# Kernel optimization log

Measured on AMD Instinct MI355X. Metric: run time of the kernel, lower is better.

The kernel has to match this reference:

```python
import jax, jax.numpy as jnp
import numpy as np

PATCH = 7
STRIDE = 1


def extract_patches(im, p=PATCH, stride=STRIDE):
    # im: [b, c, h, w] -> patches [b, N, c*p*p] (torch.nn.Unfold-style layout)
    pt = jax.lax.conv_general_dilated_patches(
        im, filter_shape=(p, p), window_strides=(stride, stride), padding='VALID')
    # pt: [b, c*p*p, h', w']
    b, d = pt.shape[0], pt.shape[1]
    return pt.reshape(b, d, -1).transpose(0, 2, 1)  # [b, N, d]


def coherence_swd(xp, yp, rand):
    # xp, yp: [N, d]; rand: [d, P]
    r = rand / jnp.std(rand, axis=0, keepdims=True, ddof=1)  # torch.std is unbiased
    px = xp @ r  # [N, P]
    py = yp @ r  # [N, P]
    ix = jnp.argsort(px, axis=0).T  # [P, N]
    iy = jnp.argsort(py, axis=0).T  # [P, N]
    # Gather full patch vectors by per-projection sorted order, L1 distance.
    # xp[ix]: [P, N, d] -- the big irregular-gather intermediate.
    diff = jnp.abs(xp[ix] - yp[iy])  # [P, N, d]
    # loss = (1/P) * sum_p mean(|...|_p); each term has identical size -> plain mean
    return diff.mean()


def setup_inputs() -> dict:
    key = jax.random.key(0)
    k1, k2, k3 = jax.random.split(key, 3)
    b, c, h, w = 1, 3, 96, 96
    d = c * PATCH * PATCH  # 147
    num_proj = 256
    x = jax.random.normal(k1, (b, c, h, w), dtype=jnp.float32)
    y = jax.random.normal(k2, (b, c, h, w), dtype=jnp.float32)
    rand = jax.random.normal(k3, (d, num_proj), dtype=jnp.float32)
    return {"x": x, "y": y, "rand": rand}


def reference(x, y, rand):
    x_patches = extract_patches(x)  # [b, N, d]
    y_patches = extract_patches(y)
    losses = jax.vmap(coherence_swd, in_axes=(0, 0, None))(x_patches, y_patches, rand)  # [b]
    return losses.mean()  # batch_reduction='mean'
```

## Files before the change

### kernel.cpp

```cpp
#include <hip/hip_runtime.h>

#define HH 96
#define WW 96
#define OH 90
#define OW 90
#define NPATCH 8100
#define DD 147
#define NPROJ 256
#define TN 64
#define KPAD 160
#define NKS 5
#define SORT_T 512
#define NBUCK 4096
#define KPT 16
#define PGRP 16
#define NCH 64
#define KPB2 128
#define QSCALE 21.25f

typedef short bf16x8 __attribute__((ext_vector_type(8)));
typedef float f32x4 __attribute__((ext_vector_type(4)));

__device__ __forceinline__ unsigned short bf16_rne(float f) {
    unsigned u = __builtin_bit_cast(unsigned, f);
    u += 0x7FFFu + ((u >> 16) & 1u);
    return (unsigned short)(u >> 16);
}
__device__ __forceinline__ float bf16_f(unsigned short h) {
    return __builtin_bit_cast(float, (unsigned)h << 16);
}

__device__ __forceinline__ unsigned sad4(unsigned x, unsigned y, unsigned a) {
    unsigned d;
    asm("v_sad_u8 %0, %1, %2, %3" : "=v"(d) : "v"(x), "v"(y), "v"(a));
    return d;
}

__global__ __launch_bounds__(512, 2)
void patch_proj_kernel(const float* __restrict__ x, const float* __restrict__ y,
                       const float* __restrict__ rnd,
                       int* __restrict__ xm8, int* __restrict__ ym8,
                       int* __restrict__ xt8, int* __restrict__ yt8,
                       float* __restrict__ pxT, float* __restrict__ pyT,
                       float* __restrict__ out)
{
    __shared__ unsigned short sh[2][TN * KPAD];
    const int tid = threadIdx.x;
    const int n0 = blockIdx.x * TN;
    const int img = blockIdx.y;
    const float* __restrict__ src = img ? y : x;
    int* __restrict__ m8 = img ? ym8 : xm8;
    int* __restrict__ t8 = img ? yt8 : xt8;
    float* __restrict__ pT = img ? pyT : pxT;
    if (blockIdx.x == 0 && img == 0 && tid == 0) out[0] = 0.0f;

    const int wv = tid >> 6, lane = tid & 63;
    const int cl = lane & 15, qk = lane >> 4;

    bf16x8 bh[NKS][2], bl[NKS][2];
#pragma unroll
    for (int ks = 0; ks < NKS; ++ks) {
#pragma unroll
        for (int nt = 0; nt < 2; ++nt) {
            const int col = wv * 32 + nt * 16 + cl;
#pragma unroll
            for (int j = 0; j < 8; ++j) {
                const int k = ks * 32 + qk * 8 + j;
                const float v = (k < DD) ? rnd[k * NPROJ + col] : 0.f;
                const unsigned short h = bf16_rne(v);
                bh[ks][nt][j] = (short)h;
                bl[ks][nt][j] = (short)bf16_rne(v - bf16_f(h));
            }
        }
    }

    for (int idx = tid; idx < TN * 40; idx += 512) {
        const int t = idx / 40;
        const int u = idx - t * 40;
        const int n = n0 + t;
        const int d0 = 4 * u;
        unsigned short h4[4], l4[4];
#pragma unroll
        for (int e = 0; e < 4; ++e) {
            const int d = d0 + e;
            float v = 0.f;
            if (n < NPATCH && d < DD) {
                const int oy = n / OW, ox = n - oy * OW;
                const int c  = d / 49, r  = d - c * 49;
                const int di = r / 7,  dj = r - di * 7;
                v = src[c * (HH * WW) + (oy + di) * WW + (ox + dj)];
            }
            const unsigned short hi = bf16_rne(v);
            h4[e] = hi;
            l4[e] = bf16_rne(v - bf16_f(hi));
        }
        const int mt = t >> 4, r16 = t & 15;
        const int ks = d0 >> 5, q = (d0 & 31) >> 3, jb = d0 & 7;
        const int fidx = (((mt * NKS + ks) * 4 + q) * 16 + r16) * 8 + jb;
        ushort4 hv; hv.x = h4[0]; hv.y = h4[1]; hv.z = h4[2]; hv.w = h4[3];
        ushort4 lv; lv.x = l4[0]; lv.y = l4[1]; lv.z = l4[2]; lv.w = l4[3];
        *(ushort4*)&sh[0][fidx] = hv;
        *(ushort4*)&sh[1][fidx] = lv;
        if (n < NPATCH) {
            unsigned w = 0;
#pragma unroll
            for (int e = 0; e < 4; ++e) {
                float f = fmaf(bf16_f(h4[e]), QSCALE, 128.5f);
                f = fminf(fmaxf(f, 0.f), 255.f);
                w |= ((unsigned)f) << (8 * e);
            }
            if (u < 32) m8[(size_t)n * 32 + u] = (int)w;
            else        t8[(size_t)n * 8 + (u - 32)] = (int)w;
        }
    }
    __syncthreads();

    f32x4 acc[4][2];
#pragma unroll
    for (int mt = 0; mt < 4; ++mt)
#pragma unroll
        for (int nt = 0; nt < 2; ++nt)
            acc[mt][nt] = (f32x4){0.f, 0.f, 0.f, 0.f};

#pragma unroll
    for (int ks = 0; ks < NKS; ++ks) {
#pragma unroll
        for (int mt = 0; mt < 4; ++mt) {
            const int base = ((mt * NKS + ks) * 64 + lane) * 8;
            const bf16x8 ah = *(const bf16x8*)&sh[0][base];
            const bf16x8 al = *(const bf16x8*)&sh[1][base];
#pragma unroll
            for (int nt = 0; nt < 2; ++nt) {
                acc[mt][nt] = __builtin_amdgcn_mfma_f32_16x16x32_bf16(ah, bh[ks][nt], acc[mt][nt], 0, 0, 0);
                acc[mt][nt] = __builtin_amdgcn_mfma_f32_16x16x32_bf16(ah, bl[ks][nt], acc[mt][nt], 0, 0, 0);
                acc[mt][nt] = __builtin_amdgcn_mfma_f32_16x16x32_bf16(al, bh[ks][nt], acc[mt][nt], 0, 0, 0);
            }
        }
    }

#pragma unroll
    for (int mt = 0; mt < 4; ++mt) {
        const int patch = n0 + mt * 16 + qk * 4;
#pragma unroll
        for (int nt = 0; nt < 2; ++nt) {
            const int proj = wv * 32 + nt * 16 + cl;
            float* rowp = pT + (size_t)proj * NPATCH + patch;
            if (patch + 3 < NPATCH) {
                *(f32x4*)rowp = acc[mt][nt];
            } else {
#pragma unroll
                for (int e = 0; e < 4; ++e)
                    if (patch + e < NPATCH) rowp[e] = acc[mt][nt][e];
            }
        }
    }
}

__global__ __launch_bounds__(SORT_T, 4)
void rank_kernel(const float* __restrict__ pT,
                 unsigned short* __restrict__ rxOut,
                 unsigned short* __restrict__ iyOut)
{
    __shared__ unsigned hist[NBUCK];
    __shared__ unsigned cnt[NBUCK];
    __shared__ float    skey[8192];
    __shared__ unsigned wsum[8];
    const int pb = blockIdx.x;
    const int tid = threadIdx.x;
    const int lane = tid & 63;
    const float* col = pT + (size_t)pb * NPATCH;

    {
        uint4 z = make_uint4(0, 0, 0, 0);
        ((uint4*)hist)[tid] = z;
        ((uint4*)hist)[tid + SORT_T] = z;
    }
    __syncthreads();

    float k[KPT];
    int bk[KPT];
#pragma unroll
    for (int t = 0; t < KPT; ++t) {
        const int i = tid + SORT_T * t;
        if (i < NPATCH) {
            const float v = col[i];
            k[t] = v;
            int b = (int)((v + 51.2f) * 40.0f);
            b = b < 0 ? 0 : (b > NBUCK - 1 ? NBUCK - 1 : b);
            bk[t] = b;
            atomicAdd(&hist[b], 1u);
        } else {
            k[t] = 0.f;
            bk[t] = -1;
        }
    }
    __syncthreads();

    {
        const int b0 = tid * 8;
        unsigned h[8];
#pragma unroll
        for (int q = 0; q < 8; ++q) h[q] = hist[b0 + q];
        unsigned tsum = 0;
#pragma unroll
        for (int q = 0; q < 8; ++q) tsum += h[q];
        unsigned acc = tsum;
#pragma unroll
        for (int d = 1; d < 64; d <<= 1) {
            const unsigned v = __shfl_up(acc, d, 64);
            if (lane >= d) acc += v;
        }
        const unsigned wexcl = acc - tsum;
        if (lane == 63) wsum[tid >> 6] = acc;
        __syncthreads();
        if (tid == 0) {
            unsigned roff = 0;
#pragma unroll
            for (int w = 0; w < 8; ++w) {
                const unsigned tt = wsum[w];
                wsum[w] = roff;
                roff += tt;
            }
        }
        __syncthreads();
        unsigned run = wsum[tid >> 6] + wexcl;
#pragma unroll
        for (int q = 0; q < 8; ++q) { cnt[b0 + q] = run; run += h[q]; }
    }
    __syncthreads();

#pragma unroll
    for (int t = 0; t < KPT; ++t) {
        if (bk[t] >= 0) {
            const unsigned pos = atomicAdd(&cnt[bk[t]], 1u);
            skey[pos] = k[t];
        }
    }
    __syncthreads();

#pragma unroll
    for (int t = 0; t < KPT; ++t) {
        const int i = tid + SORT_T * t;
        if (bk[t] < 0) continue;
        const int b = bk[t];
        const unsigned end = cnt[b];
        const unsigned cb = hist[b];
        const unsigned start = end - cb;
        const float myk = k[t];
        unsigned r = start;
        for (unsigned s2 = start; s2 < end; ++s2)
            r += (skey[s2] < myk) ? 1u : 0u;
        if (pb < NPROJ)
            rxOut[(size_t)pb * NPATCH + i] = (unsigned short)r;
        else
            iyOut[(size_t)(pb - NPROJ) * NPATCH + r] = (unsigned short)i;
    }
}

__global__ __launch_bounds__(256, 4)
void reduce_kernel(const uint4* __restrict__ xm8, const uint4* __restrict__ ym8,
                   const uint4* __restrict__ xt8, const uint4* __restrict__ yt8,
                   const unsigned short* __restrict__ rx,
                   const unsigned short* __restrict__ iy,
                   float* __restrict__ out)
{
    __shared__ unsigned short sp[PGRP * KPB2];
    const int p0 = blockIdx.y * PGRP;
    const int i0 = blockIdx.x * KPB2;
    const int iend = min(i0 + KPB2, NPATCH);
    const int tid = threadIdx.x;
    const int wave = tid >> 6, lane = tid & 63;

    for (int idx = tid; idx < PGRP * KPB2; idx += 256) {
        const int pp = idx >> 7, r = idx & 127;
        int src = i0 + r;
        src = src < NPATCH ? src : NPATCH - 1;
        const int p = p0 + pp;
        const unsigned short rk = rx[(size_t)p * NPATCH + src];
        const unsigned short j = iy[(size_t)p * NPATCH + rk];
        sp[idx] = j < NPATCH ? j : (unsigned short)(NPATCH - 1);
    }
    __syncthreads();

    unsigned uacc = 0;

    {
        const int g = lane >> 3;
        const int u = lane & 7;
#pragma unroll
        for (int it = 0; it < 4; ++it) {
            const int i = i0 + wave * 8 + it * 32;
            const uint4 xa = xm8[(size_t)i * 8 + lane];
            int jj[PGRP];
#pragma unroll
            for (int pp = 0; pp < PGRP; ++pp)
                jj[pp] = sp[pp * KPB2 + (i - i0) + g];
            uint4 ya[PGRP];
#pragma unroll
            for (int pp = 0; pp < PGRP; ++pp)
                ya[pp] = ym8[(size_t)jj[pp] * 8 + u];
            unsigned s0 = 0, s1 = 0;
#pragma unroll
            for (int pp = 0; pp < PGRP; ++pp) {
                s0 = sad4(xa.x, ya[pp].x, s0);
                s1 = sad4(xa.y, ya[pp].y, s1);
                s0 = sad4(xa.z, ya[pp].z, s0);
                s1 = sad4(xa.w, ya[pp].w, s1);
            }
            uacc += (i + g < iend) ? (s0 + s1) : 0u;
        }
    }

    {
        const int g2 = lane >> 1;
        const int u2 = lane & 1;
        const int i2 = i0 + wave * 32;
        const uint4 xa = xt8[(size_t)i2 * 2 + lane];
        int jj[PGRP];
#pragma unroll
        for (int pp = 0; pp < PGRP; ++pp)
            jj[pp] = sp[pp * KPB2 + (i2 - i0) + g2];
        uint4 ya[PGRP];
#pragma unroll
        for (int pp = 0; pp < PGRP; ++pp)
            ya[pp] = yt8[(size_t)jj[pp] * 2 + u2];
        unsigned s0 = 0, s1 = 0;
#pragma unroll
        for (int pp = 0; pp < PGRP; ++pp) {
            s0 = sad4(xa.x, ya[pp].x, s0);
            s1 = sad4(xa.y, ya[pp].y, s1);
            s0 = sad4(xa.z, ya[pp].z, s0);
            s1 = sad4(xa.w, ya[pp].w, s1);
        }
        uacc += (i2 + g2 < iend) ? (s0 + s1) : 0u;
    }

    float facc = (float)uacc;
#pragma unroll
    for (int o = 32; o > 0; o >>= 1) facc += __shfl_down(facc, o, 64);

    __shared__ float sred[4];
    if (lane == 0) sred[wave] = facc;
    __syncthreads();
    if (tid == 0) {
        const float s = sred[0] + sred[1] + sred[2] + sred[3];
        const float scale = (float)(1.0 / ((double)NPROJ * (double)NPATCH *
                                           (double)DD * (double)QSCALE));
        atomicAdd(out, s * scale);
    }
}

extern "C" void kernel_launch(void* const* d_in, const int* in_sizes, int n_in,
                              void* d_out, int out_size, void* d_ws, size_t ws_size,
                              hipStream_t stream)
{
    const float* x   = (const float*)d_in[0];
    const float* y   = (const float*)d_in[1];
    const float* rnd = (const float*)d_in[2];

    char* ws = (char*)d_ws;
    int* xm8 = (int*)(ws + 0);
    int* ym8 = (int*)(ws + 1036800);
    int* xt8 = (int*)(ws + 2073600);
    int* yt8 = (int*)(ws + 2332800);
    float* pxT = (float*)(ws + 2592000);
    float* pyT = (float*)(ws + 10886400);
    unsigned short* rx = (unsigned short*)(ws + 19180800);
    unsigned short* iy = (unsigned short*)(ws + 23328000);
    float* out = (float*)d_out;

    hipLaunchKernelGGL(patch_proj_kernel, dim3((NPATCH + TN - 1) / TN, 2), dim3(512), 0, stream,
                       x, y, rnd, xm8, ym8, xt8, yt8, pxT, pyT, out);
    hipLaunchKernelGGL(rank_kernel, dim3(2 * NPROJ), dim3(SORT_T), 0, stream,
                       pxT, rx, iy);
    hipLaunchKernelGGL(reduce_kernel, dim3(NCH, NPROJ / PGRP), dim3(256), 0, stream,
                       (const uint4*)xm8, (const uint4*)ym8,
                       (const uint4*)xt8, (const uint4*)yt8, rx, iy, out);
}
```

Baseline: 126.9 us.

## Fuse three kernels into one cooperative persistent kernel with grid syncs

Replaces the separate projection, ranking and reduction launches with a single cooperative kernel of 256 blocks that separates the phases with grid-wide syncs and reuses one shared-memory union across them. It also adds a pre-pass that converts the random projection matrix into split-bf16 transposed buffers once, instead of every projection block reconverting it. The aim is to remove launch gaps and redundant per-block conversion. In exchange, the ranking and reduction phases each loop twice per block, the kernel pays for three grid barriers, and the shared union sized for the ranking phase may limit occupancy.

```diff
diff --git a/kernel.cpp b/kernel.cpp
--- a/kernel.cpp
+++ b/kernel.cpp
@@ -1,4 +1,7 @@
 #include <hip/hip_runtime.h>
+#include <hip/hip_cooperative_groups.h>
+
+namespace cg = cooperative_groups;
 
 #define HH 96
 #define WW 96
@@ -17,6 +20,7 @@
 #define NCH 64
 #define KPB2 128
 #define QSCALE 21.25f
+#define GRID_B 256
 
 typedef short bf16x8 __attribute__((ext_vector_type(8)));
 typedef float f32x4 __attribute__((ext_vector_type(4)));
@@ -36,317 +40,335 @@
     return d;
 }
 
+union SmemU {
+    struct { unsigned short sh[2][TN * KPAD]; } a;
+    struct { unsigned hist[NBUCK]; unsigned cnt[NBUCK];
+             float skey[8192]; unsigned wsum[8]; } b;
+    struct { unsigned short sp[2][PGRP * KPB2]; float sred[2][4]; } c;
+};
+
 __global__ __launch_bounds__(512, 2)
-void patch_proj_kernel(const float* __restrict__ x, const float* __restrict__ y,
-                       const float* __restrict__ rnd,
-                       int* __restrict__ xm8, int* __restrict__ ym8,
-                       int* __restrict__ xt8, int* __restrict__ yt8,
-                       float* __restrict__ pxT, float* __restrict__ pyT,
-                       float* __restrict__ out)
+void fused_swd(const float* __restrict__ x, const float* __restrict__ y,
+               const float* __restrict__ rnd,
+               unsigned short* __restrict__ rth, unsigned short* __restrict__ rtl,
+               int* __restrict__ xm8, int* __restrict__ ym8,
+               int* __restrict__ xt8, int* __restrict__ yt8,
+               float* __restrict__ pxT, float* __restrict__ pyT,
+               unsigned short* __restrict__ rx, unsigned short* __restrict__ iy,
+               float* __restrict__ out)
 {
-    __shared__ unsigned short sh[2][TN * KPAD];
+    __shared__ SmemU smem;
+    cg::grid_group grid = cg::this_grid();
+    const int b = blockIdx.x;
     const int tid = threadIdx.x;
-    const int n0 = blockIdx.x * TN;
-    const int img = blockIdx.y;
-    const float* __restrict__ src = img ? y : x;
-    int* __restrict__ m8 = img ? ym8 : xm8;
-    int* __restrict__ t8 = img ? yt8 : xt8;
-    float* __restrict__ pT = img ? pyT : pxT;
-    if (blockIdx.x == 0 && img == 0 && tid == 0) out[0] = 0.0f;
-
     const int wv = tid >> 6, lane = tid & 63;
     const int cl = lane & 15, qk = lane >> 4;
 
-    bf16x8 bh[NKS][2], bl[NKS][2];
-#pragma unroll
-    for (int ks = 0; ks < NKS; ++ks) {
-#pragma unroll
-        for (int nt = 0; nt < 2; ++nt) {
-            const int col = wv * 32 + nt * 16 + cl;
-#pragma unroll
-            for (int j = 0; j < 8; ++j) {
-                const int k = ks * 32 + qk * 8 + j;
-                const float v = (k < DD) ? rnd[k * NPROJ + col] : 0.f;
-                const unsigned short h = bf16_rne(v);
-                bh[ks][nt][j] = (short)h;
-                bl[ks][nt][j] = (short)bf16_rne(v - bf16_f(h));
-            }
-        }
+    {
+        const int idx = b * 512 + tid;
+        if (idx < NPROJ * KPAD) {
+            const int p = idx / KPAD;
+            const int k = idx - p * KPAD;
+            const float v = (k < DD) ? rnd[k * NPROJ + p] : 0.f;
+            const unsigned short hi = bf16_rne(v);
+            rth[idx] = hi;
+            rtl[idx] = bf16_rne(v - bf16_f(hi));
+        }
+        if (b == 0 && tid == 0) out[0] = 0.0f;
     }
-
-    for (int idx = tid; idx < TN * 40; idx += 512) {
-        const int t = idx / 40;
-        const int u = idx - t * 40;
-        const int n = n0 + t;
-        const int d0 = 4 * u;
-        unsigned short h4[4], l4[4];
-#pragma unroll
-        for (int e = 0; e < 4; ++e) {
-            const int d = d0 + e;
-            float v = 0.f;
-            if (n < NPATCH && d < DD) {
-                const int oy = n / OW, ox = n - oy * OW;
-                const int c  = d / 49, r  = d - c * 49;
-                const int di = r / 7,  dj = r - di * 7;
-                v = src[c * (HH * WW) + (oy + di) * WW + (ox + dj)];
-            }
-            const unsigned short hi = bf16_rne(v);
-            h4[e] = hi;
-            l4[e] = bf16_rne(v - bf16_f(hi));
-        }
-        const int mt = t >> 4, r16 = t & 15;
-        const int ks = d0 >> 5, q = (d0 & 31) >> 3, jb = d0 & 7;
-        const int fidx = (((mt * NKS + ks) * 4 + q) * 16 + r16) * 8 + jb;
-        ushort4 hv; hv.x = h4[0]; hv.y = h4[1]; hv.z = h4[2]; hv.w = h4[3];
-        ushort4 lv; lv.x = l4[0]; lv.y = l4[1]; lv.z = l4[2]; lv.w = l4[3];
-        *(ushort4*)&sh[0][fidx] = hv;
-        *(ushort4*)&sh[1][fidx] = lv;
-        if (n < NPATCH) {
-            unsigned w = 0;
+    grid.sync();
+
+    if (b < 254) {
+        const int img = b & 1;
+        const int n0 = (b >> 1) * TN;
+        const float* __restrict__ src = img ? y : x;
+        int* __restrict__ m8 = img ? ym8 : xm8;
+        int* __restrict__ t8 = img ? yt8 : xt8;
+        float* __restrict__ pT = img ? pyT : pxT;
+
+        bf16x8 bh[NKS][2], bl[NKS][2];
+#pragma unroll
+        for (int ks = 0; ks < NKS; ++ks) {
+#pragma unroll
+            for (int nt = 0; nt < 2; ++nt) {
+                const int col = wv * 32 + nt * 16 + cl;
+                const int k0 = ks * 32 + qk * 8;
+                bh[ks][nt] = *(const bf16x8*)&rth[col * KPAD + k0];
+                bl[ks][nt] = *(const bf16x8*)&rtl[col * KPAD + k0];
+            }
+        }
+
+        for (int idx = tid; idx < TN * 40; idx += 512) {
+            const int t = idx / 40;
+            const int u = idx - t * 40;
+            const int n = n0 + t;
+            const int d0 = 4 * u;
+            unsigned short h4[4], l4[4];
 #pragma unroll
             for (int e = 0; e < 4; ++e) {
-                float f = fmaf(bf16_f(h4[e]), QSCALE, 128.5f);
-                f = fminf(fmaxf(f, 0.f), 255.f);
-                w |= ((unsigned)f) << (8 * e);
-            }
-            if (u < 32) m8[(size_t)n * 32 + u] = (int)w;
-            else        t8[(size_t)n * 8 + (u - 32)] = (int)w;
+                const int d = d0 + e;
+                float v = 0.f;
+                if (n < NPATCH && d < DD) {
+                    const int oy = n / OW, ox = n - oy * OW;
+                    const int c  = d / 49, r  = d - c * 49;
+                    const int di = r / 7,  dj = r - di * 7;
+                    v = src[c * (HH * WW) + (oy + di) * WW + (ox + dj)];
+                }
+                const unsigned short hi = bf16_rne(v);
+                h4[e] = hi;
+                l4[e] = bf16_rne(v - bf16_f(hi));
+            }
+            const int mt = t >> 4, r16 = t & 15;
+            const int ks = d0 >> 5, q = (d0 & 31) >> 3, jb = d0 & 7;
+            const int fidx = (((mt * NKS + ks) * 4 + q) * 16 + r16) * 8 + jb;
+            ushort4 hv; hv.x = h4[0]; hv.y = h4[1]; hv.z = h4[2]; hv.w = h4[3];
+            ushort4 lv; lv.x = l4[0]; lv.y = l4[1]; lv.z = l4[2]; lv.w = l4[3];
+            *(ushort4*)&smem.a.sh[0][fidx] = hv;
+            *(ushort4*)&smem.a.sh[1][fidx] = lv;
+            if (n < NPATCH) {
+                unsigned w = 0;
+#pragma unroll
+                for (int e = 0; e < 4; ++e) {
+                    float f = fmaf(bf16_f(h4[e]), QSCALE, 128.5f);
+                    f = fminf(fmaxf(f, 0.f), 255.f);
+                    w |= ((unsigned)f) << (8 * e);
+                }
+                if (u < 32) m8[(size_t)n * 32 + u] = (int)w;
+                else        t8[(size_t)n * 8 + (u - 32)] = (int)w;
+            }
+        }
+        __syncthreads();
+
+        f32x4 acc[4][2];
+#pragma unroll
+        for (int mt = 0; mt < 4; ++mt)
+#pragma unroll
+            for (int nt = 0; nt < 2; ++nt)
+                acc[mt][nt] = (f32x4){0.f, 0.f, 0.f, 0.f};
+
+#pragma unroll
+        for (int ks = 0; ks < NKS; ++ks) {
+#pragma unroll
+            for (int mt = 0; mt < 4; ++mt) {
+                const int base = ((mt * NKS + ks) * 64 + lane) * 8;
+                const bf16x8 ah = *(const bf16x8*)&smem.a.sh[0][base];
+                const bf16x8 al = *(const bf16x8*)&smem.a.sh[1][base];
+#pragma unroll
+                for (int nt = 0; nt < 2; ++nt) {
+                    acc[mt][nt] = __builtin_amdgcn_mfma_f32_16x16x32_bf16(ah, bh[ks][nt], acc[mt][nt], 0, 0, 0);
+                    acc[mt][nt] = __builtin_amdgcn_mfma_f32_16x16x32_bf16(ah, bl[ks][nt], acc[mt][nt], 0, 0, 0);
+                    acc[mt][nt] = __builtin_amdgcn_mfma_f32_16x16x32_bf16(al, bh[ks][nt], acc[mt][nt], 0, 0, 0);
+                }
+            }
+        }
+
+#pragma unroll
+        for (int mt = 0; mt < 4; ++mt) {
+            const int patch = n0 + mt * 16 + qk * 4;
+#pragma unroll
+            for (int nt = 0; nt < 2; ++nt) {
+                const int proj = wv * 32 + nt * 16 + cl;
+                float* rowp = pT + (size_t)proj * NPATCH + patch;
+                if (patch + 3 < NPATCH) {
+                    *(f32x4*)rowp = acc[mt][nt];
+                } else {
+#pragma unroll
+                    for (int e = 0; e < 4; ++e)
+                        if (patch + e < NPATCH) rowp[e] = acc[mt][nt][e];
+                }
+            }
         }
     }
-    __syncthreads();
-
-    f32x4 acc[4][2];
-#pragma unroll
-    for (int mt = 0; mt < 4; ++mt)
-#pragma unroll
-        for (int nt = 0; nt < 2; ++nt)
-            acc[mt][nt] = (f32x4){0.f, 0.f, 0.f, 0.f};
-
-#pragma unroll
-    for (int ks = 0; ks < NKS; ++ks) {
-#pragma unroll
-        for (int mt = 0; mt < 4; ++mt) {
-            const int base = ((mt * NKS + ks) * 64 + lane) * 8;
-            const bf16x8 ah = *(const bf16x8*)&sh[0][base];
-            const bf16x8 al = *(const bf16x8*)&sh[1][base];
-#pragma unroll
-            for (int nt = 0; nt < 2; ++nt) {
-                acc[mt][nt] = __builtin_amdgcn_mfma_f32_16x16x32_bf16(ah, bh[ks][nt], acc[mt][nt], 0, 0, 0);
-                acc[mt][nt] = __builtin_amdgcn_mfma_f32_16x16x32_bf16(ah, bl[ks][nt], acc[mt][nt], 0, 0, 0);
-                acc[mt][nt] = __builtin_amdgcn_mfma_f32_16x16x32_bf16(al, bh[ks][nt], acc[mt][nt], 0, 0, 0);
-            }
-        }
+    grid.sync();
+
+    for (int rep = 0; rep < 2; ++rep) {
+        const int pb = b + rep * GRID_B;
+        const float* col = pxT + (size_t)pb * NPATCH;
+
+        {
+            uint4 z = make_uint4(0, 0, 0, 0);
+            ((uint4*)smem.b.hist)[tid] = z;
+            ((uint4*)smem.b.hist)[tid + SORT_T] = z;
+        }
+        __syncthreads();
+
+        float k[KPT];
+        int bk[KPT];
+#pragma unroll
+        for (int t = 0; t < KPT; ++t) {
+            const int i = tid + SORT_T * t;
+            if (i < NPATCH) {
+                const float v = col[i];
+                k[t] = v;
+                int bq = (int)((v + 51.2f) * 40.0f);
+                bq = bq < 0 ? 0 : (bq > NBUCK - 1 ? NBUCK - 1 : bq);
+                bk[t] = bq;
+                atomicAdd(&smem.b.hist[bq], 1u);
+            } else {
+                k[t] = 0.f;
+                bk[t] = -1;
+            }
+        }
+        __syncthreads();
+
+        {
+            const int b0 = tid * 8;
+            unsigned h[8];
+#pragma unroll
+            for (int q = 0; q < 8; ++q) h[q] = smem.b.hist[b0 + q];
+            unsigned tsum = 0;
+#pragma unroll
+            for (int q = 0; q < 8; ++q) tsum += h[q];
+            unsigned acc = tsum;
+#pragma unroll
+            for (int d = 1; d < 64; d <<= 1) {
+                const unsigned v = __shfl_up(acc, d, 64);
+                if (lane >= d) acc += v;
+            }
+            const unsigned wexcl = acc - tsum;
+            if (lane == 63) smem.b.wsum[tid >> 6] = acc;
+            __syncthreads();
+            if (tid == 0) {
+                unsigned roff = 0;
+#pragma unroll
+                for (int w = 0; w < 8; ++w) {
+                    const unsigned tt = smem.b.wsum[w];
+                    smem.b.wsum[w] = roff;
+                    roff += tt;
+                }
+            }
+            __syncthreads();
+            unsigned run = smem.b.wsum[tid >> 6] + wexcl;
+#pragma unroll
+            for (int q = 0; q < 8; ++q) { smem.b.cnt[b0 + q] = run; run += h[q]; }
+        }
+        __syncthreads();
+
+#pragma unroll
+        for (int t = 0; t < KPT; ++t) {
+            if (bk[t] >= 0) {
+                const unsigned pos = atomicAdd(&smem.b.cnt[bk[t]], 1u);
+                smem.b.skey[pos] = k[t];
+            }
+        }
+        __syncthreads();
+
+#pragma unroll
+        for (int t = 0; t < KPT; ++t) {
+            const int i = tid + SORT_T * t;
+            if (bk[t] < 0) continue;
+            const int bq = bk[t];
+            const unsigned end = smem.b.cnt[bq];
+            const unsigned cb = smem.b.hist[bq];
+            const unsigned start = end - cb;
+            const float myk = k[t];
+            unsigned r = start;
+            for (unsigned s2 = start; s2 < end; ++s2)
+                r += (smem.b.skey[s2] < myk) ? 1u : 0u;
+            if (pb < NPROJ)
+                rx[(size_t)pb * NPATCH + i] = (unsigned short)r;
+            else
+                iy[(size_t)(pb - NPROJ) * NPATCH + r] = (unsigned short)i;
+        }
+        __syncthreads();
     }
-
-#pragma unroll
-    for (int mt = 0; mt < 4; ++mt) {
-        const int patch = n0 + mt * 16 + qk * 4;
-#pragma unroll
-        for (int nt = 0; nt < 2; ++nt) {
-            const int proj = wv * 32 + nt * 16 + cl;
-            float* rowp = pT + (size_t)proj * NPATCH + patch;
-            if (patch + 3 < NPATCH) {
-                *(f32x4*)rowp = acc[mt][nt];
-            } else {
-#pragma unroll
-                for (int e = 0; e < 4; ++e)
-                    if (patch + e < NPATCH) rowp[e] = acc[mt][nt][e];
-            }
-        }
-    }
-}
-
-__global__ __launch_bounds__(SORT_T, 4)
-void rank_kernel(const float* __restrict__ pT,
-                 unsigned short* __restrict__ rxOut,
-                 unsigned short* __restrict__ iyOut)
-{
-    __shared__ unsigned hist[NBUCK];
-    __shared__ unsigned cnt[NBUCK];
-    __shared__ float    skey[8192];
-    __shared__ unsigned wsum[8];
-    const int pb = blockIdx.x;
-    const int tid = threadIdx.x;
-    const int lane = tid & 63;
-    const float* col = pT + (size_t)pb * NPATCH;
+    grid.sync();
 
     {
-        uint4 z = make_uint4(0, 0, 0, 0);
-        ((uint4*)hist)[tid] = z;
-        ((uint4*)hist)[tid + SORT_T] = z;
-    }
-    __syncthreads();
-
-    float k[KPT];
-    int bk[KPT];
-#pragma unroll
-    for (int t = 0; t < KPT; ++t) {
-        const int i = tid + SORT_T * t;
-        if (i < NPATCH) {
-            const float v = col[i];
-            k[t] = v;
-            int b = (int)((v + 51.2f) * 40.0f);
-            b = b < 0 ? 0 : (b > NBUCK - 1 ? NBUCK - 1 : b);
-            bk[t] = b;
-            atomicAdd(&hist[b], 1u);
-        } else {
-            k[t] = 0.f;
-            bk[t] = -1;
-        }
-    }
-    __syncthreads();
-
-    {
-        const int b0 = tid * 8;
-        unsigned h[8];
-#pragma unroll
-        for (int q = 0; q < 8; ++q) h[q] = hist[b0 + q];
-        unsigned tsum = 0;
-#pragma unroll
-        for (int q = 0; q < 8; ++q) tsum += h[q];
-        unsigned acc = tsum;
-#pragma unroll
-        for (int d = 1; d < 64; d <<= 1) {
-            const unsigned v = __shfl_up(acc, d, 64);
-            if (lane >= d) acc += v;
-        }
-        const unsigned wexcl = acc - tsum;
-        if (lane == 63) wsum[tid >> 6] = acc;
-        __syncthreads();
-        if (tid == 0) {
-            unsigned roff = 0;
-#pragma unroll
-            for (int w = 0; w < 8; ++w) {
-                const unsigned tt = wsum[w];
-                wsum[w] = roff;
-                roff += tt;
-            }
-        }
-        __syncthreads();
-        unsigned run = wsum[tid >> 6] + wexcl;
-#pragma unroll
-        for (int q = 0; q < 8; ++q) { cnt[b0 + q] = run; run += h[q]; }
-    }
-    __syncthreads();
-
-#pragma unroll
-    for (int t = 0; t < KPT; ++t) {
-        if (bk[t] >= 0) {
-            const unsigned pos = atomicAdd(&cnt[bk[t]], 1u);
-            skey[pos] = k[t];
-        }
-    }
-    __syncthreads();
-
-#pragma unroll
-    for (int t = 0; t < KPT; ++t) {
-        const int i = tid + SORT_T * t;
-        if (bk[t] < 0) continue;
-        const int b = bk[t];
-        const unsigned end = cnt[b];
-        const unsigned cb = hist[b];
-        const unsigned start = end - cb;
-        const float myk = k[t];
-        unsigned r = start;
-        for (unsigned s2 = start; s2 < end; ++s2)
-            r += (skey[s2] < myk) ? 1u : 0u;
-        if (pb < NPROJ)
-            rxOut[(size_t)pb * NPATCH + i] = (unsigned short)r;
-        else
-            iyOut[(size_t)(pb - NPROJ) * NPATCH + r] = (unsigned short)i;
-    }
-}
-
-__global__ __launch_bounds__(256, 4)
-void reduce_kernel(const uint4* __restrict__ xm8, const uint4* __restrict__ ym8,
-                   const uint4* __restrict__ xt8, const uint4* __restrict__ yt8,
-                   const unsigned short* __restrict__ rx,
-                   const unsigned short* __restrict__ iy,
-                   float* __restrict__ out)
-{
-    __shared__ unsigned short sp[PGRP * KPB2];
-    const int p0 = blockIdx.y * PGRP;
-    const int i0 = blockIdx.x * KPB2;
-    const int iend = min(i0 + KPB2, NPATCH);
-    const int tid = threadIdx.x;
-    const int wave = tid >> 6, lane = tid & 63;
-
-    for (int idx = tid; idx < PGRP * KPB2; idx += 256) {
-        const int pp = idx >> 7, r = idx & 127;
-        int src = i0 + r;
-        src = src < NPATCH ? src : NPATCH - 1;
-        const int p = p0 + pp;
-        const unsigned short rk = rx[(size_t)p * NPATCH + src];
-        const unsigned short j = iy[(size_t)p * NPATCH + rk];
-        sp[idx] = j < NPATCH ? j : (unsigned short)(NPATCH - 1);
-    }
-    __syncthreads();
-
-    unsigned uacc = 0;
-
-    {
-        const int g = lane >> 3;
-        const int u = lane & 7;
-#pragma unroll
-        for (int it = 0; it < 4; ++it) {
-            const int i = i0 + wave * 8 + it * 32;
-            const uint4 xa = xm8[(size_t)i * 8 + lane];
-            int jj[PGRP];
-#pragma unroll
-            for (int pp = 0; pp < PGRP; ++pp)
-                jj[pp] = sp[pp * KPB2 + (i - i0) + g];
-            uint4 ya[PGRP];
-#pragma unroll
-            for (int pp = 0; pp < PGRP; ++pp)
-                ya[pp] = ym8[(size_t)jj[pp] * 8 + u];
-            unsigned s0 = 0, s1 = 0;
-#pragma unroll
-            for (int pp = 0; pp < PGRP; ++pp) {
-                s0 = sad4(xa.x, ya[pp].x, s0);
-                s1 = sad4(xa.y, ya[pp].y, s1);
-                s0 = sad4(xa.z, ya[pp].z, s0);
-                s1 = sad4(xa.w, ya[pp].w, s1);
-            }
-            uacc += (i + g < iend) ? (s0 + s1) : 0u;
-        }
-    }
-
-    {
-        const int g2 = lane >> 1;
-        const int u2 = lane & 1;
-        const int i2 = i0 + wave * 32;
-        const uint4 xa = xt8[(size_t)i2 * 2 + lane];
-        int jj[PGRP];
-#pragma unroll
-        for (int pp = 0; pp < PGRP; ++pp)
-            jj[pp] = sp[pp * KPB2 + (i2 - i0) + g2];
-        uint4 ya[PGRP];
-#pragma unroll
-        for (int pp = 0; pp < PGRP; ++pp)
-            ya[pp] = yt8[(size_t)jj[pp] * 2 + u2];
-        unsigned s0 = 0, s1 = 0;
-#pragma unroll
-        for (int pp = 0; pp < PGRP; ++pp) {
-            s0 = sad4(xa.x, ya[pp].x, s0);
-            s1 = sad4(xa.y, ya[pp].y, s1);
-            s0 = sad4(xa.z, ya[pp].z, s0);
-            s1 = sad4(xa.w, ya[pp].w, s1);
-        }
-        uacc += (i2 + g2 < iend) ? (s0 + s1) : 0u;
-    }
-
-    float facc = (float)uacc;
-#pragma unroll
-    for (int o = 32; o > 0; o >>= 1) facc += __shfl_down(facc, o, 64);
-
-    __shared__ float sred[4];
-    if (lane == 0) sred[wave] = facc;
-    __syncthreads();
-    if (tid == 0) {
-        const float s = sred[0] + sred[1] + sred[2] + sred[3];
-        const float scale = (float)(1.0 / ((double)NPROJ * (double)NPATCH *
-                                           (double)DD * (double)QSCALE));
-        atomicAdd(out, s * scale);
+        const uint4* __restrict__ xm = (const uint4*)xm8;
+        const uint4* __restrict__ ym = (const uint4*)ym8;
+        const uint4* __restrict__ xt = (const uint4*)xt8;
+        const uint4* __restrict__ yt = (const uint4*)yt8;
+        const int half = tid >> 8;
+        const int t2 = tid & 255;
+        const int wave = t2 >> 6, ln = t2 & 63;
+        unsigned short* sp = smem.c.sp[half];
+
+        for (int rep = 0; rep < 2; ++rep) {
+            const int vb = ((b << 1) | half) + (rep << 9);
+            const int i0 = (vb & 63) * KPB2;
+            const int p0 = (vb >> 6) * PGRP;
+            const int iend = min(i0 + KPB2, NPATCH);
+
+            for (int idx = t2; idx < PGRP * KPB2; idx += 256) {
+                const int pp = idx >> 7, r = idx & 127;
+                int src = i0 + r;
+                src = src < NPATCH ? src : NPATCH - 1;
+                const int p = p0 + pp;
+                const unsigned short rk = rx[(size_t)p * NPATCH + src];
+                const unsigned short j = iy[(size_t)p * NPATCH + rk];
+                sp[idx] = j < NPATCH ? j : (unsigned short)(NPATCH - 1);
+            }
+            __syncthreads();
+
+            unsigned uacc = 0;
+
+            {
+                const int g = ln >> 3;
+                const int u = ln & 7;
+#pragma unroll
+                for (int it = 0; it < 4; ++it) {
+                    const int i = i0 + wave * 8 + it * 32;
+                    const uint4 xa = xm[(size_t)i * 8 + ln];
+                    int jj[PGRP];
+#pragma unroll
+                    for (int pp = 0; pp < PGRP; ++pp)
+                        jj[pp] = sp[pp * KPB2 + (i - i0) + g];
+                    uint4 ya[PGRP];
+#pragma unroll
+                    for (int pp = 0; pp < PGRP; ++pp)
+                        ya[pp] = ym[(size_t)jj[pp] * 8 + u];
+                    unsigned s0 = 0, s1 = 0;
+#pragma unroll
+                    for (int pp = 0; pp < PGRP; ++pp) {
+                        s0 = sad4(xa.x, ya[pp].x, s0);
+                        s1 = sad4(xa.y, ya[pp].y, s1);
+                        s0 = sad4(xa.z, ya[pp].z, s0);
+                        s1 = sad4(xa.w, ya[pp].w, s1);
+                    }
+                    uacc += (i + g < iend) ? (s0 + s1) : 0u;
+                }
+            }
+
+            {
+                const int g2 = ln >> 1;
+                const int u2 = ln & 1;
+                const int i2 = i0 + wave * 32;
+                const uint4 xa = xt[(size_t)i2 * 2 + ln];
+                int jj[PGRP];
+#pragma unroll
+                for (int pp = 0; pp < PGRP; ++pp)
+                    jj[pp] = sp[pp * KPB2 + (i2 - i0) + g2];
+                uint4 ya[PGRP];
+#pragma unroll
+                for (int pp = 0; pp < PGRP; ++pp)
+                    ya[pp] = yt[(size_t)jj[pp] * 2 + u2];
+                unsigned s0 = 0, s1 = 0;
+#pragma unroll
+                for (int pp = 0; pp < PGRP; ++pp) {
+                    s0 = sad4(xa.x, ya[pp].x, s0);
+                    s1 = sad4(xa.y, ya[pp].y, s1);
+                    s0 = sad4(xa.z, ya[pp].z, s0);
+                    s1 = sad4(xa.w, ya[pp].w, s1);
+                }
+                uacc += (i2 + g2 < iend) ? (s0 + s1) : 0u;
+            }
+
+            float facc = (float)uacc;
+#pragma unroll
+            for (int o = 32; o > 0; o >>= 1) facc += __shfl_down(facc, o, 64);
+
+            if (ln == 0) smem.c.sred[half][wave] = facc;
+            __syncthreads();
+            if (t2 == 0) {
+                const float s = smem.c.sred[half][0] + smem.c.sred[half][1] +
+                                smem.c.sred[half][2] + smem.c.sred[half][3];
+                const float scale = (float)(1.0 / ((double)NPROJ * (double)NPATCH *
+                                                   (double)DD * (double)QSCALE));
+                atomicAdd(out, s * scale);
+            }
+            __syncthreads();
+        }
     }
 }
 
@@ -367,13 +389,18 @@
     float* pyT = (float*)(ws + 10886400);
     unsigned short* rx = (unsigned short*)(ws + 19180800);
     unsigned short* iy = (unsigned short*)(ws + 23328000);
+    unsigned short* rth = (unsigned short*)(ws + 27475200);
+    unsigned short* rtl = (unsigned short*)(ws + 27557120);
     float* out = (float*)d_out;
 
-    hipLaunchKernelGGL(patch_proj_kernel, dim3((NPATCH + TN - 1) / TN, 2), dim3(512), 0, stream,
-                       x, y, rnd, xm8, ym8, xt8, yt8, pxT, pyT, out);
-    hipLaunchKernelGGL(rank_kernel, dim3(2 * NPROJ), dim3(SORT_T), 0, stream,
-                       pxT, rx, iy);
-    hipLaunchKernelGGL(reduce_kernel, dim3(NCH, NPROJ / PGRP), dim3(256), 0, stream,
-                       (const uint4*)xm8, (const uint4*)ym8,
-                       (const uint4*)xt8, (const uint4*)yt8, rx, iy, out);
+    void* args[] = {
+        (void*)&x, (void*)&y, (void*)&rnd,
+        (void*)&rth, (void*)&rtl,
+        (void*)&xm8, (void*)&ym8, (void*)&xt8, (void*)&yt8,
+        (void*)&pxT, (void*)&pyT,
+        (void*)&rx, (void*)&iy,
+        (void*)&out
+    };
+    hipLaunchCooperativeKernel((const void*)fused_swd, dim3(GRID_B), dim3(512),
+                               args, 0, stream);
 }
```

New measurement: 259.9 us. 2.05x slower.

## Fuse x and y rank passes per projection and emit partner indices directly

Applied to the files above, without the earlier changes.

Each rank block now sorts both the x and y projection columns for one projection in two passes. It builds the inverse permutation of y in shared memory and writes a single partner-index array, so the separate rank and inverse arrays and the reduce kernel's dependent double gather go away. The block grows to 1024 threads with 8 keys per thread, which halves the grid to 256 blocks and adds shared memory for the inverse table. That lowers parallelism and may limit occupancy, since only 256 blocks fill the machine.

```diff
diff --git a/kernel.cpp b/kernel.cpp
--- a/kernel.cpp
+++ b/kernel.cpp
@@ -10,9 +10,9 @@
 #define TN 64
 #define KPAD 160
 #define NKS 5
-#define SORT_T 512
+#define SORT_T 1024
 #define NBUCK 4096
-#define KPT 16
+#define KPT 8
 #define PGRP 16
 #define NCH 64
 #define KPB2 128
@@ -158,110 +158,127 @@
 
 __global__ __launch_bounds__(SORT_T, 4)
 void rank_kernel(const float* __restrict__ pT,
-                 unsigned short* __restrict__ rxOut,
-                 unsigned short* __restrict__ iyOut)
+                 unsigned short* __restrict__ partner)
 {
     __shared__ unsigned hist[NBUCK];
     __shared__ unsigned cnt[NBUCK];
     __shared__ float    skey[8192];
-    __shared__ unsigned wsum[8];
-    const int pb = blockIdx.x;
+    __shared__ unsigned short iyl[8192];
+    __shared__ unsigned wsum[16];
+    const int p = blockIdx.x;
     const int tid = threadIdx.x;
     const int lane = tid & 63;
-    const float* col = pT + (size_t)pb * NPATCH;
-
-    {
-        uint4 z = make_uint4(0, 0, 0, 0);
-        ((uint4*)hist)[tid] = z;
-        ((uint4*)hist)[tid + SORT_T] = z;
-    }
-    __syncthreads();
-
-    float k[KPT];
-    int bk[KPT];
+    const int wid = tid >> 6;
+
+    unsigned short xr[KPT];
+
+#pragma unroll
+    for (int pass = 0; pass < 2; ++pass) {
+        const float* col = pT + (size_t)(p + pass * NPROJ) * NPATCH;
+
+        ((uint4*)hist)[tid] = make_uint4(0, 0, 0, 0);
+        ((uint4*)cnt)[tid]  = make_uint4(0, 0, 0, 0);
+        if (pass == 1) {
+            ((uint4*)iyl)[tid] = make_uint4(0xFFFFFFFFu, 0xFFFFFFFFu,
+                                            0xFFFFFFFFu, 0xFFFFFFFFu);
+            if (tid < 1024) ((uint4*)iyl)[tid + 1024] = make_uint4(
+                0xFFFFFFFFu, 0xFFFFFFFFu, 0xFFFFFFFFu, 0xFFFFFFFFu);
+        }
+        __syncthreads();
+
+        float k[KPT];
+        int bk[KPT];
+#pragma unroll
+        for (int t = 0; t < KPT; ++t) {
+            const int i = tid + SORT_T * t;
+            if (i < NPATCH) {
+                const float v = col[i];
+                k[t] = v;
+                int b = (int)((v + 51.2f) * 40.0f);
+                b = b < 0 ? 0 : (b > NBUCK - 1 ? NBUCK - 1 : b);
+                bk[t] = b;
+                atomicAdd(&hist[b], 1u);
+            } else {
+                k[t] = 0.f;
+                bk[t] = -1;
+            }
+        }
+        __syncthreads();
+
+        {
+            const int b0 = tid * 4;
+            unsigned h[4];
+#pragma unroll
+            for (int q = 0; q < 4; ++q) h[q] = hist[b0 + q];
+            unsigned tsum = h[0] + h[1] + h[2] + h[3];
+            unsigned acc = tsum;
+#pragma unroll
+            for (int d = 1; d < 64; d <<= 1) {
+                const unsigned v = __shfl_up(acc, d, 64);
+                if (lane >= d) acc += v;
+            }
+            const unsigned wexcl = acc - tsum;
+            if (lane == 63) wsum[wid] = acc;
+            __syncthreads();
+            if (tid == 0) {
+                unsigned roff = 0;
+#pragma unroll
+                for (int w = 0; w < 16; ++w) {
+                    const unsigned tt = wsum[w];
+                    wsum[w] = roff;
+                    roff += tt;
+                }
+            }
+            __syncthreads();
+            unsigned run = wsum[wid] + wexcl;
+#pragma unroll
+            for (int q = 0; q < 4; ++q) { cnt[b0 + q] = run; run += h[q]; }
+        }
+        __syncthreads();
+
+#pragma unroll
+        for (int t = 0; t < KPT; ++t) {
+            if (bk[t] >= 0) {
+                const unsigned pos = atomicAdd(&cnt[bk[t]], 1u);
+                skey[pos] = k[t];
+            }
+        }
+        __syncthreads();
+
+#pragma unroll
+        for (int t = 0; t < KPT; ++t) {
+            if (bk[t] < 0) continue;
+            const int b = bk[t];
+            const unsigned end = cnt[b];
+            const unsigned cb = hist[b];
+            const unsigned start = end - cb;
+            const float myk = k[t];
+            unsigned r = start;
+            for (unsigned s2 = start; s2 < end; ++s2)
+                r += (skey[s2] < myk) ? 1u : 0u;
+            if (pass == 0) {
+                xr[t] = (unsigned short)r;
+            } else {
+                iyl[r] = (unsigned short)(tid + SORT_T * t);
+            }
+        }
+        __syncthreads();
+    }
+
 #pragma unroll
     for (int t = 0; t < KPT; ++t) {
         const int i = tid + SORT_T * t;
-        if (i < NPATCH) {
-            const float v = col[i];
-            k[t] = v;
-            int b = (int)((v + 51.2f) * 40.0f);
-            b = b < 0 ? 0 : (b > NBUCK - 1 ? NBUCK - 1 : b);
-            bk[t] = b;
-            atomicAdd(&hist[b], 1u);
-        } else {
-            k[t] = 0.f;
-            bk[t] = -1;
-        }
-    }
-    __syncthreads();
-
-    {
-        const int b0 = tid * 8;
-        unsigned h[8];
-#pragma unroll
-        for (int q = 0; q < 8; ++q) h[q] = hist[b0 + q];
-        unsigned tsum = 0;
-#pragma unroll
-        for (int q = 0; q < 8; ++q) tsum += h[q];
-        unsigned acc = tsum;
-#pragma unroll
-        for (int d = 1; d < 64; d <<= 1) {
-            const unsigned v = __shfl_up(acc, d, 64);
-            if (lane >= d) acc += v;
-        }
-        const unsigned wexcl = acc - tsum;
-        if (lane == 63) wsum[tid >> 6] = acc;
-        __syncthreads();
-        if (tid == 0) {
-            unsigned roff = 0;
-#pragma unroll
-            for (int w = 0; w < 8; ++w) {
-                const unsigned tt = wsum[w];
-                wsum[w] = roff;
-                roff += tt;
-            }
-        }
-        __syncthreads();
-        unsigned run = wsum[tid >> 6] + wexcl;
-#pragma unroll
-        for (int q = 0; q < 8; ++q) { cnt[b0 + q] = run; run += h[q]; }
-    }
-    __syncthreads();
-
-#pragma unroll
-    for (int t = 0; t < KPT; ++t) {
-        if (bk[t] >= 0) {
-            const unsigned pos = atomicAdd(&cnt[bk[t]], 1u);
-            skey[pos] = k[t];
-        }
-    }
-    __syncthreads();
-
-#pragma unroll
-    for (int t = 0; t < KPT; ++t) {
-        const int i = tid + SORT_T * t;
-        if (bk[t] < 0) continue;
-        const int b = bk[t];
-        const unsigned end = cnt[b];
-        const unsigned cb = hist[b];
-        const unsigned start = end - cb;
-        const float myk = k[t];
-        unsigned r = start;
-        for (unsigned s2 = start; s2 < end; ++s2)
-            r += (skey[s2] < myk) ? 1u : 0u;
-        if (pb < NPROJ)
-            rxOut[(size_t)pb * NPATCH + i] = (unsigned short)r;
-        else
-            iyOut[(size_t)(pb - NPROJ) * NPATCH + r] = (unsigned short)i;
+        if (i >= NPATCH) continue;
+        const unsigned short j = iyl[xr[t]];
+        partner[(size_t)p * NPATCH + i] =
+            (j < NPATCH) ? j : (unsigned short)(NPATCH - 1);
     }
 }
 
 __global__ __launch_bounds__(256, 4)
 void reduce_kernel(const uint4* __restrict__ xm8, const uint4* __restrict__ ym8,
                    const uint4* __restrict__ xt8, const uint4* __restrict__ yt8,
-                   const unsigned short* __restrict__ rx,
-                   const unsigned short* __restrict__ iy,
+                   const unsigned short* __restrict__ partner,
                    float* __restrict__ out)
 {
     __shared__ unsigned short sp[PGRP * KPB2];
@@ -275,10 +292,7 @@
         const int pp = idx >> 7, r = idx & 127;
         int src = i0 + r;
         src = src < NPATCH ? src : NPATCH - 1;
-        const int p = p0 + pp;
-        const unsigned short rk = rx[(size_t)p * NPATCH + src];
-        const unsigned short j = iy[(size_t)p * NPATCH + rk];
-        sp[idx] = j < NPATCH ? j : (unsigned short)(NPATCH - 1);
+        sp[idx] = partner[(size_t)(p0 + pp) * NPATCH + src];
     }
     __syncthreads();
 
@@ -365,15 +379,14 @@
     int* yt8 = (int*)(ws + 2332800);
     float* pxT = (float*)(ws + 2592000);
     float* pyT = (float*)(ws + 10886400);
-    unsigned short* rx = (unsigned short*)(ws + 19180800);
-    unsigned short* iy = (unsigned short*)(ws + 23328000);
+    unsigned short* partner = (unsigned short*)(ws + 19180800);
     float* out = (float*)d_out;
 
     hipLaunchKernelGGL(patch_proj_kernel, dim3((NPATCH + TN - 1) / TN, 2), dim3(512), 0, stream,
                        x, y, rnd, xm8, ym8, xt8, yt8, pxT, pyT, out);
-    hipLaunchKernelGGL(rank_kernel, dim3(2 * NPROJ), dim3(SORT_T), 0, stream,
-                       pxT, rx, iy);
+    hipLaunchKernelGGL(rank_kernel, dim3(NPROJ), dim3(SORT_T), 0, stream,
+                       pxT, partner);
     hipLaunchKernelGGL(reduce_kernel, dim3(NCH, NPROJ / PGRP), dim3(256), 0, stream,
                        (const uint4*)xm8, (const uint4*)ym8,
-                       (const uint4*)xt8, (const uint4*)yt8, rx, iy, out);
-}
+                       (const uint4*)xt8, (const uint4*)yt8, partner, out);
+}
```

New measurement: 120.1 us. 1.06x faster.
